# Optimization experiments

Hardware: AMD Instinct MI355X
Metric: run time of the kernel (lower is better)

Reference implementation:

```python
import jax, jax.numpy as jnp
import numpy as np

N = 16_777_216  # total elements
B = 16_384      # number of segments (graphs/batches)
EPS = 1e-12


def setup_inputs() -> dict:
    key = jax.random.key(0)
    k1, k2, k3 = jax.random.split(key, 3)
    preds = jax.random.normal(k1, (N,), dtype=jnp.float32)
    target = jax.random.normal(k2, (N,), dtype=jnp.float32)
    batch_map = jnp.sort(jax.random.randint(k3, (N,), 0, B, dtype=jnp.int64))
    return {"preds": preds, "target": target, "batch_map": batch_map}


def reference(preds, target, batch_map):
    # per-segment squared norms and dot product (three scatter-sums in torch)
    seg = lambda v: jax.ops.segment_sum(v, batch_map, num_segments=B,
                                        indices_are_sorted=True)
    preds_norm = jnp.sqrt(seg(preds * preds))      # [B]
    target_norm = jnp.sqrt(seg(target * target))   # [B]
    dot_product = seg(preds * target)              # [B]
    cosine = dot_product / jnp.maximum(preds_norm * target_norm, EPS)
    return jnp.mean(1.0 - cosine)
```

## Files before the change

kernel.cpp:

```cpp
#include <hip/hip_runtime.h>

#define NSEG 16384
#define EPS 1e-12f

__global__ void bsearch_kernel(const int* __restrict__ map,
                               int* __restrict__ start, int n) {
    int b = blockIdx.x * blockDim.x + threadIdx.x;
    if (b > NSEG) return;
    int est = b << 10;
    int wlo = est - 20000; if (wlo < 0) wlo = 0;
    int whi = est + 20000; if (whi > n) whi = n;
    int lo = wlo, hi = whi;
    while (lo < hi) { int mid = (lo + hi) >> 1; if (map[mid] < b) lo = mid + 1; else hi = mid; }
    bool bad = (lo == wlo && wlo > 0 && map[wlo - 1] >= b) ||
               (lo == whi && whi < n && map[whi] < b);
    if (bad) {
        lo = 0; hi = n;
        while (lo < hi) { int mid = (lo + hi) >> 1; if (map[mid] < b) lo = mid + 1; else hi = mid; }
    }
    start[b] = lo;
}

#define REDUCE3(x, y, z)                                   \
    do {                                                   \
        _Pragma("unroll")                                  \
        for (int off_ = 32; off_ > 0; off_ >>= 1) {        \
            x += __shfl_down(x, off_);                     \
            y += __shfl_down(y, off_);                     \
            z += __shfl_down(z, off_);                     \
        }                                                  \
    } while (0)

__global__ __launch_bounds__(256) void seg_main(const float4* __restrict__ p4,
                                                const float4* __restrict__ t4,
                                                const int* __restrict__ map,
                                                const int* __restrict__ start,
                                                float4* __restrict__ wb) {
    const int wid  = threadIdx.x >> 6;
    const int lane = threadIdx.x & 63;
    const int w     = blockIdx.x * 4 + wid;
    const int ebase = w << 11;
    const int vbase = w << 9;

    float4 P[8], T[8];
    #pragma unroll
    for (int k = 0; k < 8; ++k) P[k] = p4[vbase + lane + k * 64];
    #pragma unroll
    for (int k = 0; k < 8; ++k) T[k] = t4[vbase + lane + k * 64];

    int mv = 0;
    if (lane < 2) mv = map[ebase + lane * 2047];
    const int mfirst = __shfl(mv, 0);
    const int mlast  = __shfl(mv, 1);
    const int nloc   = mlast - mfirst;

    int sv = 0;
    if (lane < 4) { int q = mfirst + lane; if (q > NSEG) q = NSEG; sv = start[q]; }
    const int sfirst = __shfl(sv, 0);
    const int b1     = __shfl(sv, 1);
    const int b2     = __shfl(sv, 2);
    const int b3     = __shfl(sv, 3);

    float a0 = 0, a1 = 0, a2 = 0, a3 = 0;
    float c0 = 0, c1 = 0, c2 = 0, c3 = 0;
    float d0 = 0, d1 = 0, d2 = 0, d3 = 0;

    if (nloc == 1) {
        #pragma unroll
        for (int k = 0; k < 8; ++k) {
            const int u = ebase + ((lane + k * 64) << 2);
            const float4 pv = P[k], tv = T[k];
            #define ACC2(pe, te, idx)                                      \
            {   float xx = (pe) * (pe), yy = (te) * (te), xy = (pe) * (te);\
                bool cnd = (idx) < b1;                                     \
                a0 += cnd ? xx : 0.0f; c0 += cnd ? yy : 0.0f; d0 += cnd ? xy : 0.0f; \
                a1 += cnd ? 0.0f : xx; c1 += cnd ? 0.0f : yy; d1 += cnd ? 0.0f : xy; }
            ACC2(pv.x, tv.x, u + 0)
            ACC2(pv.y, tv.y, u + 1)
            ACC2(pv.z, tv.z, u + 2)
            ACC2(pv.w, tv.w, u + 3)
            #undef ACC2
        }
    } else {
        #pragma unroll
        for (int k = 0; k < 8; ++k) {
            const int u = ebase + ((lane + k * 64) << 2);
            const float4 pv = P[k], tv = T[k];
            #define ACC4(pe, te, idx)                                      \
            {   float xx = (pe) * (pe), yy = (te) * (te), xy = (pe) * (te);\
                bool g1 = (idx) >= b1, g2 = (idx) >= b2, g3 = (idx) >= b3; \
                float m0 = g1 ? 0.0f : 1.0f;                               \
                float m1 = (g1 && !g2) ? 1.0f : 0.0f;                      \
                float m2 = (g2 && !g3) ? 1.0f : 0.0f;                      \
                float m3 = g3 ? 1.0f : 0.0f;                               \
                a0 += xx * m0; c0 += yy * m0; d0 += xy * m0;               \
                a1 += xx * m1; c1 += yy * m1; d1 += xy * m1;               \
                a2 += xx * m2; c2 += yy * m2; d2 += xy * m2;               \
                a3 += xx * m3; c3 += yy * m3; d3 += xy * m3; }
            ACC4(pv.x, tv.x, u + 0)
            ACC4(pv.y, tv.y, u + 1)
            ACC4(pv.z, tv.z, u + 2)
            ACC4(pv.w, tv.w, u + 3)
            #undef ACC4
        }
    }

    REDUCE3(a0, c0, d0);
    REDUCE3(a1, c1, d1);
    if (nloc >= 2) REDUCE3(a2, c2, d2);
    if (nloc >= 3) REDUCE3(a3, c3, d3);

    if (lane == 0) {
        const int src0 = w - (sfirst >> 11);
        wb[mfirst * 2 + src0] = make_float4(a0, c0, d0, 0.0f);
        if (nloc >= 1) wb[(mfirst + 1) * 2] = make_float4(a1, c1, d1, 0.0f);
        if (nloc >= 2) wb[(mfirst + 2) * 2] = make_float4(a2, c2, d2, 0.0f);
        if (nloc >= 3) wb[(mfirst + 3) * 2] = make_float4(a3, c3, d3, 0.0f);
    }
}

__global__ void finalize1(const float4* __restrict__ wb,
                          const int* __restrict__ start,
                          float* __restrict__ part) {
    float local = 0.0f;
    for (int s = blockIdx.x * blockDim.x + threadIdx.x; s < NSEG;
         s += gridDim.x * blockDim.x) {
        const int s0 = start[s], s1 = start[s + 1];
        float cosv = 0.0f;
        if (s1 > s0) {
            float4 v = wb[s * 2];
            const int r0 = s0 >> 11, r1 = (s1 - 1) >> 11;
            if (r1 > r0) {
                float4 u2 = wb[s * 2 + 1];
                v.x += u2.x; v.y += u2.y; v.z += u2.z;
            }
            cosv = v.z / fmaxf(sqrtf(v.x) * sqrtf(v.y), EPS);
        }
        local += 1.0f - cosv;
    }
    #pragma unroll
    for (int off = 32; off > 0; off >>= 1) local += __shfl_down(local, off);
    __shared__ float wsum[4];
    const int wid = threadIdx.x >> 6;
    if ((threadIdx.x & 63) == 0) wsum[wid] = local;
    __syncthreads();
    if (threadIdx.x == 0)
        part[blockIdx.x] = wsum[0] + wsum[1] + wsum[2] + wsum[3];
}

__global__ void finalize2(const float* __restrict__ part,
                          float* __restrict__ out, int npart) {
    float local = (threadIdx.x < npart) ? part[threadIdx.x] : 0.0f;
    #pragma unroll
    for (int off = 32; off > 0; off >>= 1) local += __shfl_down(local, off);
    if (threadIdx.x == 0) out[0] = local / (float)NSEG;
}

extern "C" void kernel_launch(void* const* d_in, const int* in_sizes, int n_in,
                              void* d_out, int out_size, void* d_ws, size_t ws_size,
                              hipStream_t stream) {
    const float4* p = (const float4*)d_in[0];
    const float4* t = (const float4*)d_in[1];
    const int*    s = (const int*)d_in[2];
    const int n = in_sizes[0];

    int*    start = (int*)d_ws;
    float4* wb    = (float4*)((char*)d_ws + 66048);
    float*  part  = (float*)((char*)d_ws + 66048 + 524288);

    bsearch_kernel<<<(NSEG + 1 + 255) / 256, 256, 0, stream>>>(s, start, n);
    seg_main<<<2048, 256, 0, stream>>>(p, t, s, start, wb);
    finalize1<<<64, 256, 0, stream>>>(wb, start, part);
    finalize2<<<1, 64, 0, stream>>>(part, (float*)d_out, 64);
}
```

Before: 39.05 us.

## Split wave work into half-chunks with uniform fast paths and ballot segment lookup

Each wave's 2048-element chunk is now handled as two 1024-element halves. A 256-element group that lies entirely inside one segment takes a uniform fast path with no per-element masking; only groups that straddle a boundary fall back to per-element selects. Segment IDs are found by a ballot over a window of precomputed start offsets, so the kernel no longer reads batch_map. The partial-sum buffer grows to three slots per segment, and the finalize kernel is updated to combine up to three partials.

```diff
diff --git a/kernel.cpp b/kernel.cpp
--- a/kernel.cpp
+++ b/kernel.cpp
@@ -1,7 +1,7 @@
 #include <hip/hip_runtime.h>
 
 #define NSEG 16384
-#define EPS 1e-12f
+#define EPS  1e-12f
 
 __global__ void bsearch_kernel(const int* __restrict__ map,
                                int* __restrict__ start, int n) {
@@ -21,102 +21,108 @@
     start[b] = lo;
 }
 
-#define REDUCE3(x, y, z)                                   \
-    do {                                                   \
-        _Pragma("unroll")                                  \
-        for (int off_ = 32; off_ > 0; off_ >>= 1) {        \
-            x += __shfl_down(x, off_);                     \
-            y += __shfl_down(y, off_);                     \
-            z += __shfl_down(z, off_);                     \
-        }                                                  \
+#define REDUCE3(x, y, z)                              \
+    do {                                              \
+        _Pragma("unroll")                             \
+        for (int off_ = 32; off_ > 0; off_ >>= 1) {   \
+            x += __shfl_down(x, off_);                \
+            y += __shfl_down(y, off_);                \
+            z += __shfl_down(z, off_);                \
+        }                                             \
+    } while (0)
+
+#define COL(pe, te, eidx)                                                       \
+    { const float px_ = (pe), tx_ = (te);                                       \
+      const float cxx_ = px_ * px_, cyy_ = tx_ * tx_, cxy_ = px_ * tx_;         \
+      const bool i0_ = (eidx) < bb1_;                                           \
+      const bool i2_ = (eidx) >= bb2_;                                          \
+      a0 += i0_ ? cxx_ : 0.f; c0 += i0_ ? cyy_ : 0.f; d0 += i0_ ? cxy_ : 0.f;   \
+      a2 += i2_ ? cxx_ : 0.f; c2 += i2_ ? cyy_ : 0.f; d2 += i2_ ? cxy_ : 0.f;   \
+      const bool i1_ = !i0_ && !i2_;                                            \
+      a1 += i1_ ? cxx_ : 0.f; c1 += i1_ ? cyy_ : 0.f; d1 += i1_ ? cxy_ : 0.f; }
+
+#define DO_HALF(P, T, HBASE, MH, SFIRST, B1, B2, CC)                            \
+    do {                                                                        \
+        float a0=0,c0=0,d0=0, a1=0,c1=0,d1=0, a2=0,c2=0,d2=0;                   \
+        const int bb1_ = (B1), bb2_ = (B2);                                     \
+        const int hend_ = (HBASE) + 1024;                                       \
+        _Pragma("unroll")                                                       \
+        for (int g_ = 0; g_ < 4; ++g_) {                                        \
+            const float4 pv = P[g_], tv = T[g_];                                \
+            const int G_  = (HBASE) + g_ * 256;                                 \
+            const int Ge_ = G_ + 256;                                           \
+            if (Ge_ <= bb1_) {                                                  \
+                a0 += pv.x*pv.x + pv.y*pv.y + pv.z*pv.z + pv.w*pv.w;            \
+                c0 += tv.x*tv.x + tv.y*tv.y + tv.z*tv.z + tv.w*tv.w;            \
+                d0 += pv.x*tv.x + pv.y*tv.y + pv.z*tv.z + pv.w*tv.w;            \
+            } else if (G_ >= bb1_ && Ge_ <= bb2_) {                             \
+                a1 += pv.x*pv.x + pv.y*pv.y + pv.z*pv.z + pv.w*pv.w;            \
+                c1 += tv.x*tv.x + tv.y*tv.y + tv.z*tv.z + tv.w*tv.w;            \
+                d1 += pv.x*tv.x + pv.y*tv.y + pv.z*tv.z + pv.w*tv.w;            \
+            } else if (G_ >= bb2_) {                                            \
+                a2 += pv.x*pv.x + pv.y*pv.y + pv.z*pv.z + pv.w*pv.w;            \
+                c2 += tv.x*tv.x + tv.y*tv.y + tv.z*tv.z + tv.w*tv.w;            \
+                d2 += pv.x*tv.x + pv.y*tv.y + pv.z*tv.z + pv.w*tv.w;            \
+            } else {                                                            \
+                const int e0_ = (HBASE) + (g_ * 64 + lane) * 4;                 \
+                COL(pv.x, tv.x, e0_ + 0)                                        \
+                COL(pv.y, tv.y, e0_ + 1)                                        \
+                COL(pv.z, tv.z, e0_ + 2)                                        \
+                COL(pv.w, tv.w, e0_ + 3)                                        \
+            }                                                                   \
+        }                                                                       \
+        const int nloc_ = (bb1_ < hend_) + (bb2_ < hend_);                      \
+        REDUCE3(a0, c0, d0);                                                    \
+        if (nloc_ >= 1) REDUCE3(a1, c1, d1);                                    \
+        if (nloc_ >= 2) REDUCE3(a2, c2, d2);                                    \
+        if (lane == 0) {                                                        \
+            wb[(MH) * 3 + ((CC) - ((SFIRST) >> 10))] = make_float4(a0, c0, d0, 0.f); \
+            if (nloc_ >= 1) wb[((MH) + 1) * 3] = make_float4(a1, c1, d1, 0.f);  \
+            if (nloc_ >= 2) wb[((MH) + 2) * 3] = make_float4(a2, c2, d2, 0.f);  \
+        }                                                                       \
     } while (0)
 
 __global__ __launch_bounds__(256) void seg_main(const float4* __restrict__ p4,
                                                 const float4* __restrict__ t4,
-                                                const int* __restrict__ map,
                                                 const int* __restrict__ start,
                                                 float4* __restrict__ wb) {
-    const int wid  = threadIdx.x >> 6;
     const int lane = threadIdx.x & 63;
+    const int wid  = __builtin_amdgcn_readfirstlane(threadIdx.x >> 6);
     const int w     = blockIdx.x * 4 + wid;
     const int ebase = w << 11;
     const int vbase = w << 9;
 
-    float4 P[8], T[8];
+    const int base_id = (ebase >> 10) - 20;
+    int gidx = base_id + lane;
+    gidx = gidx < 0 ? 0 : (gidx > NSEG ? NSEG : gidx);
+    const int sv = start[gidx];
+
+    float4 PA[4], TA[4], PB[4], TB[4];
     #pragma unroll
-    for (int k = 0; k < 8; ++k) P[k] = p4[vbase + lane + k * 64];
+    for (int k = 0; k < 4; ++k) PA[k] = p4[vbase + k * 64 + lane];
     #pragma unroll
-    for (int k = 0; k < 8; ++k) T[k] = t4[vbase + lane + k * 64];
+    for (int k = 0; k < 4; ++k) TA[k] = t4[vbase + k * 64 + lane];
+    #pragma unroll
+    for (int k = 0; k < 4; ++k) PB[k] = p4[vbase + 256 + k * 64 + lane];
+    #pragma unroll
+    for (int k = 0; k < 4; ++k) TB[k] = t4[vbase + 256 + k * 64 + lane];
 
-    int mv = 0;
-    if (lane < 2) mv = map[ebase + lane * 2047];
-    const int mfirst = __shfl(mv, 0);
-    const int mlast  = __shfl(mv, 1);
-    const int nloc   = mlast - mfirst;
+    const unsigned long long m0 = __ballot(sv <= ebase);
+    const int k0 = 63 - __builtin_clzll(m0);
+    const unsigned long long m1 = __ballot(sv <= ebase + 1024);
+    const int k1 = 63 - __builtin_clzll(m1);
 
-    int sv = 0;
-    if (lane < 4) { int q = mfirst + lane; if (q > NSEG) q = NSEG; sv = start[q]; }
-    const int sfirst = __shfl(sv, 0);
-    const int b1     = __shfl(sv, 1);
-    const int b2     = __shfl(sv, 2);
-    const int b3     = __shfl(sv, 3);
+    const int mh0 = base_id + k0;
+    const int mh1 = base_id + k1;
+    const int s00 = __builtin_amdgcn_readlane(sv, k0);
+    const int b01 = __builtin_amdgcn_readlane(sv, k0 + 1 > 63 ? 63 : k0 + 1);
+    const int b02 = __builtin_amdgcn_readlane(sv, k0 + 2 > 63 ? 63 : k0 + 2);
+    const int s10 = __builtin_amdgcn_readlane(sv, k1);
+    const int b11 = __builtin_amdgcn_readlane(sv, k1 + 1 > 63 ? 63 : k1 + 1);
+    const int b12 = __builtin_amdgcn_readlane(sv, k1 + 2 > 63 ? 63 : k1 + 2);
 
-    float a0 = 0, a1 = 0, a2 = 0, a3 = 0;
-    float c0 = 0, c1 = 0, c2 = 0, c3 = 0;
-    float d0 = 0, d1 = 0, d2 = 0, d3 = 0;
-
-    if (nloc == 1) {
-        #pragma unroll
-        for (int k = 0; k < 8; ++k) {
-            const int u = ebase + ((lane + k * 64) << 2);
-            const float4 pv = P[k], tv = T[k];
-            #define ACC2(pe, te, idx)                                      \
-            {   float xx = (pe) * (pe), yy = (te) * (te), xy = (pe) * (te);\
-                bool cnd = (idx) < b1;                                     \
-                a0 += cnd ? xx : 0.0f; c0 += cnd ? yy : 0.0f; d0 += cnd ? xy : 0.0f; \
-                a1 += cnd ? 0.0f : xx; c1 += cnd ? 0.0f : yy; d1 += cnd ? 0.0f : xy; }
-            ACC2(pv.x, tv.x, u + 0)
-            ACC2(pv.y, tv.y, u + 1)
-            ACC2(pv.z, tv.z, u + 2)
-            ACC2(pv.w, tv.w, u + 3)
-            #undef ACC2
-        }
-    } else {
-        #pragma unroll
-        for (int k = 0; k < 8; ++k) {
-            const int u = ebase + ((lane + k * 64) << 2);
-            const float4 pv = P[k], tv = T[k];
-            #define ACC4(pe, te, idx)                                      \
-            {   float xx = (pe) * (pe), yy = (te) * (te), xy = (pe) * (te);\
-                bool g1 = (idx) >= b1, g2 = (idx) >= b2, g3 = (idx) >= b3; \
-                float m0 = g1 ? 0.0f : 1.0f;                               \
-                float m1 = (g1 && !g2) ? 1.0f : 0.0f;                      \
-                float m2 = (g2 && !g3) ? 1.0f : 0.0f;                      \
-                float m3 = g3 ? 1.0f : 0.0f;                               \
-                a0 += xx * m0; c0 += yy * m0; d0 += xy * m0;               \
-                a1 += xx * m1; c1 += yy * m1; d1 += xy * m1;               \
-                a2 += xx * m2; c2 += yy * m2; d2 += xy * m2;               \
-                a3 += xx * m3; c3 += yy * m3; d3 += xy * m3; }
-            ACC4(pv.x, tv.x, u + 0)
-            ACC4(pv.y, tv.y, u + 1)
-            ACC4(pv.z, tv.z, u + 2)
-            ACC4(pv.w, tv.w, u + 3)
-            #undef ACC4
-        }
-    }
-
-    REDUCE3(a0, c0, d0);
-    REDUCE3(a1, c1, d1);
-    if (nloc >= 2) REDUCE3(a2, c2, d2);
-    if (nloc >= 3) REDUCE3(a3, c3, d3);
-
-    if (lane == 0) {
-        const int src0 = w - (sfirst >> 11);
-        wb[mfirst * 2 + src0] = make_float4(a0, c0, d0, 0.0f);
-        if (nloc >= 1) wb[(mfirst + 1) * 2] = make_float4(a1, c1, d1, 0.0f);
-        if (nloc >= 2) wb[(mfirst + 2) * 2] = make_float4(a2, c2, d2, 0.0f);
-        if (nloc >= 3) wb[(mfirst + 3) * 2] = make_float4(a3, c3, d3, 0.0f);
-    }
+    DO_HALF(PA, TA, ebase,        mh0, s00, b01, b02, (w << 1));
+    DO_HALF(PB, TB, ebase + 1024, mh1, s10, b11, b12, (w << 1) + 1);
 }
 
 __global__ void finalize1(const float4* __restrict__ wb,
@@ -128,12 +134,10 @@
         const int s0 = start[s], s1 = start[s + 1];
         float cosv = 0.0f;
         if (s1 > s0) {
-            float4 v = wb[s * 2];
-            const int r0 = s0 >> 11, r1 = (s1 - 1) >> 11;
-            if (r1 > r0) {
-                float4 u2 = wb[s * 2 + 1];
-                v.x += u2.x; v.y += u2.y; v.z += u2.z;
-            }
+            float4 v = wb[s * 3];
+            const int r0 = s0 >> 10, r1 = (s1 - 1) >> 10;
+            if (r1 > r0)     { float4 u = wb[s * 3 + 1]; v.x += u.x; v.y += u.y; v.z += u.z; }
+            if (r1 > r0 + 1) { float4 u = wb[s * 3 + 2]; v.x += u.x; v.y += u.y; v.z += u.z; }
             cosv = v.z / fmaxf(sqrtf(v.x) * sqrtf(v.y), EPS);
         }
         local += 1.0f - cosv;
@@ -141,8 +145,8 @@
     #pragma unroll
     for (int off = 32; off > 0; off >>= 1) local += __shfl_down(local, off);
     __shared__ float wsum[4];
-    const int wid = threadIdx.x >> 6;
-    if ((threadIdx.x & 63) == 0) wsum[wid] = local;
+    const int wd = threadIdx.x >> 6;
+    if ((threadIdx.x & 63) == 0) wsum[wd] = local;
     __syncthreads();
     if (threadIdx.x == 0)
         part[blockIdx.x] = wsum[0] + wsum[1] + wsum[2] + wsum[3];
@@ -165,11 +169,11 @@
     const int n = in_sizes[0];
 
     int*    start = (int*)d_ws;
-    float4* wb    = (float4*)((char*)d_ws + 66048);
-    float*  part  = (float*)((char*)d_ws + 66048 + 524288);
+    float4* wb    = (float4*)((char*)d_ws + 65552);
+    float*  part  = (float*)((char*)d_ws + 65552 + 786432);
 
-    bsearch_kernel<<<(NSEG + 1 + 255) / 256, 256, 0, stream>>>(s, start, n);
-    seg_main<<<2048, 256, 0, stream>>>(p, t, s, start, wb);
+    bsearch_kernel<<<65, 256, 0, stream>>>(s, start, n);
+    seg_main<<<2048, 256, 0, stream>>>(p, t, start, wb);
     finalize1<<<64, 256, 0, stream>>>(wb, start, part);
     finalize2<<<1, 64, 0, stream>>>(part, (float*)d_out, 64);
 }
```

Result: no change. 38.31 us (-1.9%).
